# Kernel optimization log

Measured on AMD Instinct MI355X. Metric: run time of the kernel, lower is better.

The kernel has to match this reference:

```python
import jax, jax.numpy as jnp
import numpy as np

NUM_HEADS = 16

def setup_inputs() -> dict:
    key = jax.random.key(0)
    ks = jax.random.split(key, 6)
    S, B, D = 2048, 4, 1280
    return {
        "hidden_states": jax.random.normal(ks[0], (S, B, D), dtype=jnp.float32),
        "rotary_pos_emb": jax.random.normal(ks[1], (S, D // NUM_HEADS // 2), dtype=jnp.float32),
        "in_proj_w": jax.random.normal(ks[2], (3 * D, D), dtype=jnp.float32) * 0.02,
        "in_proj_b": jax.random.normal(ks[3], (3 * D,), dtype=jnp.float32) * 0.02,
        "out_proj_w": jax.random.normal(ks[4], (D, D), dtype=jnp.float32) * 0.02,
        "out_proj_b": jax.random.normal(ks[5], (D,), dtype=jnp.float32) * 0.02,
    }

def _rotate_half(x):
    h = x.shape[-1] // 2
    return jnp.concatenate([-x[..., h:], x[..., :h]], axis=-1)

def _apply_rope(t, cos, sin):
    # t: [B,S,H,Dh]; cos/sin: [1,S,1,Dh]. Compute in fp32 like the original.
    orig = t.dtype
    t32 = t.astype(jnp.float32)
    return (t32 * cos + _rotate_half(t32) * sin).astype(orig)

def reference(hidden_states, rotary_pos_emb, in_proj_w, in_proj_b, out_proj_w, out_proj_b):
    S, B, D = hidden_states.shape
    H = NUM_HEADS
    Dh = D // H

    # Fused QKV projection: [S,B,3D]
    qkv = jnp.einsum('sbd,ed->sbe', hidden_states, in_proj_w) + in_proj_b
    qkv = qkv.reshape(S, B, 3, H, Dh).transpose(2, 1, 0, 3, 4)  # [3,B,S,H,Dh]
    q, k, v = qkv[0], qkv[1], qkv[2]

    # RoPE tables: freqs [S, Dh/2] -> tiled to [1,S,1,Dh] (repeat along last dim)
    cos = jnp.tile(jnp.cos(rotary_pos_emb), (1, 2))[None, :, None, :].astype(jnp.float32)
    sin = jnp.tile(jnp.sin(rotary_pos_emb), (1, 2))[None, :, None, :].astype(jnp.float32)
    q = _apply_rope(q, cos, sin)
    k = _apply_rope(k, cos, sin)

    # [B,H,S,Dh]
    q = q.transpose(0, 2, 1, 3)
    k = k.transpose(0, 2, 1, 3)
    v = v.transpose(0, 2, 1, 3)

    scale = 1.0 / np.sqrt(Dh).astype(np.float32)
    scores = jnp.einsum('bhqd,bhkd->bhqk', q, k) * scale
    attn = jax.nn.softmax(scores, axis=-1)
    out = jnp.einsum('bhqk,bhkd->bhqd', attn, v)  # [B,H,S,Dh]

    out = out.transpose(2, 0, 1, 3).reshape(S, B, D)  # [S,B,D]
    return jnp.einsum('sbd,ed->sbe', out, out_proj_w) + out_proj_b
```

## Files before the change

### kernel.cpp

```cpp
#include <hip/hip_runtime.h>
#include <hip/hip_bf16.h>
#include <math.h>

typedef __bf16 bf16x4 __attribute__((ext_vector_type(4)));
typedef __bf16 bf16x8 __attribute__((ext_vector_type(8)));
typedef float  f32x4  __attribute__((ext_vector_type(4)));

#define S_LEN 2048
#define BATCH 4
#define DMODEL 1280
#define NHEAD 16
#define DHEAD 80
#define KDIM 1280

__device__ __forceinline__ f32x4 mfma_bf16(bf16x8 a, bf16x8 b, f32x4 c) {
  return __builtin_amdgcn_mfma_f32_16x16x32_bf16(a, b, c, 0, 0, 0);
}

__device__ __forceinline__ void gload16(const void* g, void* l) {
  __builtin_amdgcn_global_load_lds(
      (const __attribute__((address_space(1))) unsigned int*)g,
      (__attribute__((address_space(3))) unsigned int*)l, 16, 0, 0);
}

__global__ void cast_f32_to_bf16(const float* __restrict__ in,
                                 __bf16* __restrict__ out, int n4) {
  int i = blockIdx.x * 256 + threadIdx.x;
  if (i >= n4) return;
  float4 v = reinterpret_cast<const float4*>(in)[i];
  bf16x4 o;
  o[0] = (__bf16)v.x; o[1] = (__bf16)v.y; o[2] = (__bf16)v.z; o[3] = (__bf16)v.w;
  reinterpret_cast<bf16x4*>(out)[i] = o;
}

__global__ void build_sincos(const float* __restrict__ rot,
                             float* __restrict__ ctab, float* __restrict__ stab, int n) {
  int i = blockIdx.x * 256 + threadIdx.x;
  if (i >= n) return;
  float v = rot[i];
  ctab[i] = cosf(v);
  stab[i] = sinf(v);
}

__global__ void zero_fill(float* __restrict__ p, int n) {
  int i = blockIdx.x * 256 + threadIdx.x;
  if (i < n) p[i] = 0.0f;
}

__global__ __launch_bounds__(512, 2) void gemm256_qkv(
    const __bf16* __restrict__ A, const __bf16* __restrict__ Bw,
    const float* __restrict__ bias,
    __bf16* __restrict__ qw, __bf16* __restrict__ kw, __bf16* __restrict__ vtw)
{
  __shared__ __align__(1024) char smem[2][65536];
  const int tid = threadIdx.x;
  const int lane = tid & 63;
  const int w = tid >> 6;
  const int lr = lane & 15, lg = lane >> 4;
  const int wr = w >> 2, wc = w & 3;

  const int wg = blockIdx.x;
  const int xcd = wg & 7, idx = wg >> 3;
  const int bx = xcd * 4 + (idx & 3);
  const int by = idx >> 2;
  const int r0 = bx * 256, c0 = by * 256;
  const char* asrc = (const char*)(A + (size_t)r0 * KDIM);
  const char* bsrc = (const char*)(Bw + (size_t)c0 * KDIM);

  f32x4 acc[8][4] = {};

  auto stage = [&](int buf, int kt) {
    const size_t kb = (size_t)kt * 128;
#pragma unroll
    for (int i = 0; i < 8; ++i) {
      const int L = i * 8192 + tid * 16;
      const int r = (L & 32767) >> 7;
      const int coff = (L & 127) ^ ((r & 7) << 4);
      const char* s = (i < 4 ? asrc : bsrc) + (size_t)r * 2560 + kb + coff;
      gload16(s, &smem[buf][L]);
    }
  };

  auto compute = [&](int buf) {
#pragma unroll
    for (int kk = 0; kk < 2; ++kk) {
      bf16x8 af[8], bfr[4];
#pragma unroll
      for (int rt = 0; rt < 8; ++rt) {
        const int row = wr * 128 + rt * 16 + lr;
        af[rt] = *reinterpret_cast<const bf16x8*>(
            &smem[buf][row * 128 + ((kk * 64 + lg * 16) ^ ((row & 7) << 4))]);
      }
#pragma unroll
      for (int ct = 0; ct < 4; ++ct) {
        const int row = wc * 64 + ct * 16 + lr;
        bfr[ct] = *reinterpret_cast<const bf16x8*>(
            &smem[buf][32768 + row * 128 + ((kk * 64 + lg * 16) ^ ((row & 7) << 4))]);
      }
#pragma unroll
      for (int rt = 0; rt < 8; ++rt)
#pragma unroll
        for (int ct = 0; ct < 4; ++ct)
          acc[rt][ct] = mfma_bf16(af[rt], bfr[ct], acc[rt][ct]);
    }
  };

  stage(0, 0);
  asm volatile("s_waitcnt vmcnt(0)" ::: "memory");
  __builtin_amdgcn_s_barrier();
  __builtin_amdgcn_sched_barrier(0);

  for (int t = 0; t < 20; ++t) {
    const int buf = t & 1;
    if (t < 19) stage(buf ^ 1, t + 1);
    compute(buf);
    __builtin_amdgcn_sched_barrier(0);
    asm volatile("s_waitcnt vmcnt(0)" ::: "memory");
    __builtin_amdgcn_sched_barrier(0);
    __builtin_amdgcn_s_barrier();
    __builtin_amdgcn_sched_barrier(0);
  }

  const int which = c0 / DMODEL;
  float biasr[4];
#pragma unroll
  for (int ct = 0; ct < 4; ++ct) biasr[ct] = bias[c0 + wc * 64 + ct * 16 + lr];

#pragma unroll
  for (int ct = 0; ct < 4; ++ct) {
    const int c = c0 + wc * 64 + ct * 16 + lr;
    const int ee = c - which * DMODEL;
    const int h = ee / DHEAD;
    const int dh = ee - h * DHEAD;
#pragma unroll
    for (int rt = 0; rt < 8; ++rt)
#pragma unroll
      for (int j = 0; j < 4; ++j) {
        const int r = r0 + wr * 128 + rt * 16 + lg * 4 + j;
        const int s = r >> 2, b = r & 3;
        const __bf16 bv = (__bf16)(acc[rt][ct][j] + biasr[ct]);
        if (which == 0)
          qw[((size_t)(b * NHEAD + h) * S_LEN + s) * DHEAD + dh] = bv;
        else if (which == 1)
          kw[((size_t)(b * NHEAD + h) * S_LEN + s) * DHEAD + dh] = bv;
        else {
          const int sp = (s & ~31) | ((s & 12) << 1) | ((s & 16) >> 2) | (s & 3);
          vtw[((size_t)(b * NHEAD + h) * DHEAD + dh) * S_LEN + sp] = bv;
        }
      }
  }
}

template <int MODE>
__global__ __launch_bounds__(256) void gemm_bt(
    const __bf16* __restrict__ A, const __bf16* __restrict__ Bw,
    const float* __restrict__ bias, float* __restrict__ outf)
{
  __shared__ __align__(16) char smem[2][2][16384];
  const int tid = threadIdx.x;
  const int lane = tid & 63;
  const int w = tid >> 6;
  const int lr = lane & 15, lg = lane >> 4;
  const int rowblk = (w >> 1) * 64, colblk = (w & 1) * 64;
  const int sxz = (lane & 7) << 4;

  const int wg = blockIdx.x;
  const int xcd = wg & 7, idx = wg >> 3;
  const int bx = xcd * 8 + (idx & 7);
  const int by = idx >> 3;
  const int r0 = bx * 128;
  const int c0 = by * 128;
  const char* asrc = (const char*)(A + (size_t)r0 * KDIM);
  const char* bsrc = (const char*)(Bw + (size_t)c0 * KDIM);

  f32x4 acc[4][4] = {};

  auto stage = [&](int buf, int kt) {
    const size_t kb = (size_t)kt * 128;
#pragma unroll
    for (int i = 0; i < 4; ++i) {
      int L = i * 4096 + tid * 16;
      int r = L >> 7;
      int coff = (L & 127) ^ ((r & 7) << 4);
      gload16(asrc + (size_t)r * 2560 + kb + coff, &smem[buf][0][L]);
      gload16(bsrc + (size_t)r * 2560 + kb + coff, &smem[buf][1][L]);
    }
  };

  auto compute = [&](int buf) {
#pragma unroll
    for (int kk = 0; kk < 2; ++kk) {
      const int cb = (kk * 64 + lg * 16) ^ sxz;
      bf16x8 af[4], bfr[4];
#pragma unroll
      for (int rf = 0; rf < 4; ++rf)
        af[rf] = *reinterpret_cast<const bf16x8*>(&smem[buf][0][(rowblk + rf * 16 + lr) * 128 + cb]);
#pragma unroll
      for (int cf = 0; cf < 4; ++cf)
        bfr[cf] = *reinterpret_cast<const bf16x8*>(&smem[buf][1][(colblk + cf * 16 + lr) * 128 + cb]);
#pragma unroll
      for (int rf = 0; rf < 4; ++rf)
#pragma unroll
        for (int cf = 0; cf < 4; ++cf)
          acc[rf][cf] = mfma_bf16(af[rf], bfr[cf], acc[rf][cf]);
    }
  };

  stage(0, 0);
  asm volatile("s_waitcnt vmcnt(0)" ::: "memory");
  __builtin_amdgcn_s_barrier();
  __builtin_amdgcn_sched_barrier(0);

  for (int t = 0; t < 20; ++t) {
    const int buf = t & 1;
    if (t < 19) {
      stage(buf ^ 1, t + 1);
      asm volatile("s_waitcnt vmcnt(8)" ::: "memory");
    } else {
      asm volatile("s_waitcnt vmcnt(0)" ::: "memory");
    }
    __builtin_amdgcn_sched_barrier(0);
    __builtin_amdgcn_s_barrier();
    __builtin_amdgcn_sched_barrier(0);

    compute(buf);

    __builtin_amdgcn_sched_barrier(0);
    __builtin_amdgcn_s_barrier();
    __builtin_amdgcn_sched_barrier(0);
  }

  float biasr[4];
#pragma unroll
  for (int cf = 0; cf < 4; ++cf) biasr[cf] = bias[c0 + colblk + cf * 16 + lr];

#pragma unroll
  for (int rf = 0; rf < 4; ++rf)
#pragma unroll
    for (int cf = 0; cf < 4; ++cf) {
      const int c = c0 + colblk + cf * 16 + lr;
#pragma unroll
      for (int j = 0; j < 4; ++j) {
        const int r = r0 + rowblk + rf * 16 + lg * 4 + j;
        outf[(size_t)r * DMODEL + c] = acc[rf][cf][j] + biasr[cf];
      }
    }
}

__global__ void rope_kernel(__bf16* __restrict__ qw, __bf16* __restrict__ kw,
                            const float* __restrict__ ctab, const float* __restrict__ stab,
                            float qscale)
{
  int idx = blockIdx.x * 256 + threadIdx.x;
  const int j = idx % 10;
  int rest = idx / 10;
  const int s = rest & (S_LEN - 1);
  rest >>= 11;
  const int bh = rest & 63;
  const int isk = rest >> 6;
  __bf16* base = (isk ? kw : qw) + ((size_t)bh * S_LEN + s) * DHEAD;
  const float4 c4 = *reinterpret_cast<const float4*>(ctab + s * 40 + j * 4);
  const float4 s4 = *reinterpret_cast<const float4*>(stab + s * 40 + j * 4);
  bf16x4 a = *reinterpret_cast<bf16x4*>(base + j * 4);
  bf16x4 b = *reinterpret_cast<bf16x4*>(base + 40 + j * 4);
  const float m = isk ? 1.0f : qscale;
  const float cc[4] = {c4.x, c4.y, c4.z, c4.w};
  const float ss[4] = {s4.x, s4.y, s4.z, s4.w};
#pragma unroll
  for (int t = 0; t < 4; ++t) {
    float fa = (float)a[t], fb = (float)b[t];
    a[t] = (__bf16)((fa * cc[t] - fb * ss[t]) * m);
    b[t] = (__bf16)((fb * cc[t] + fa * ss[t]) * m);
  }
  *reinterpret_cast<bf16x4*>(base + j * 4) = a;
  *reinterpret_cast<bf16x4*>(base + 40 + j * 4) = b;
}

__global__ __launch_bounds__(256, 3) void attn_kernel(
    const __bf16* __restrict__ qw, const __bf16* __restrict__ kw,
    const __bf16* __restrict__ vtw, __bf16* __restrict__ ow,
    const float* __restrict__ zp)
{
  __shared__ __align__(1024) char smem[2][24576];

  const int tid = threadIdx.x;
  const int lane = tid & 63;
  const int w = tid >> 6;
  const int lr = lane & 15, lg = lane >> 4;

  const int wg = blockIdx.x;
  const int local = wg >> 3;
  const int bh = (wg & 7) * 8 + (local >> 4);
  const int qt = local & 15;

  const char* qbase = (const char*)(qw + ((size_t)bh * S_LEN + qt * 128) * DHEAD);
  const char* kbase = (const char*)(kw + (size_t)bh * S_LEN * DHEAD);
  const char* vbase = (const char*)(vtw + (size_t)bh * DHEAD * S_LEN);
  const char* zpb = (const char*)zp;

  bf16x8 z8, one8;
#pragma unroll
  for (int i = 0; i < 8; ++i) { z8[i] = (__bf16)0.0f; one8[i] = (__bf16)1.0f; }

  bf16x8 aq[2][3];
#pragma unroll
  for (int m = 0; m < 2; ++m) {
    const char* rp = qbase + (size_t)(w * 32 + m * 16 + lr) * 160;
    aq[m][0] = *reinterpret_cast<const bf16x8*>(rp + lg * 16);
    aq[m][1] = *reinterpret_cast<const bf16x8*>(rp + 64 + lg * 16);
    aq[m][2] = (lg < 2) ? *reinterpret_cast<const bf16x8*>(rp + 128 + lg * 16) : z8;
  }

  const char* src[6];
  size_t step[6];
#pragma unroll
  for (int i = 0; i < 6; ++i) {
    const int s = w * 6 + i;
    if (s < 12) {
      const int ks = s >> 2, n = s & 3;
      if (ks == 2 && lg >= 2) { src[i] = zpb + lane * 16; step[i] = 0; }
      else { src[i] = kbase + (size_t)(n * 16 + lr) * 160 + ks * 64 + lg * 16; step[i] = 64 * 160; }
    } else {
      const int v = s - 12, mf = v >> 1, ks2 = v & 1;
      if (mf == 5) { src[i] = zpb + lane * 16; step[i] = 0; }
      else { src[i] = vbase + (size_t)(mf * 16 + lr) * 4096 + (size_t)(ks2 * 32 + lg * 8) * 2; step[i] = 128; }
    }
  }

  auto stage = [&](int buf) {
#pragma unroll
    for (int i = 0; i < 6; ++i) {
      gload16(src[i], &smem[buf][(w * 6 + i) * 1024]);
      src[i] += step[i];
    }
  };

  f32x4 accO[5][2] = {};
  f32x4 accD[2] = {};

  stage(0);
  asm volatile("s_waitcnt vmcnt(0)" ::: "memory");
  __builtin_amdgcn_s_barrier();
  __builtin_amdgcn_sched_barrier(0);

  for (int t = 0; t < 32; ++t) {
    const int buf = t & 1;
    if (t < 31) {
      stage(buf ^ 1);
      asm volatile("s_waitcnt vmcnt(6)" ::: "memory");
    } else {
      asm volatile("s_waitcnt vmcnt(0)" ::: "memory");
    }
    __builtin_amdgcn_sched_barrier(0);
    __builtin_amdgcn_s_barrier();
    __builtin_amdgcn_sched_barrier(0);

    const char* Kb = smem[buf];
    const char* Vb = smem[buf] + 12288;

    f32x4 sc[2][4] = {};
#pragma unroll
    for (int n = 0; n < 4; ++n) {
      bf16x8 af0 = *reinterpret_cast<const bf16x8*>(Kb + (0 * 4 + n) * 1024 + lane * 16);
      bf16x8 af1 = *reinterpret_cast<const bf16x8*>(Kb + (1 * 4 + n) * 1024 + lane * 16);
      bf16x8 af2 = *reinterpret_cast<const bf16x8*>(Kb + (2 * 4 + n) * 1024 + lane * 16);
#pragma unroll
      for (int m = 0; m < 2; ++m) {
        sc[m][n] = mfma_bf16(af0, aq[m][0], sc[m][n]);
        sc[m][n] = mfma_bf16(af1, aq[m][1], sc[m][n]);
        sc[m][n] = mfma_bf16(af2, aq[m][2], sc[m][n]);
      }
    }

    bf16x8 bp[2][2];
#pragma unroll
    for (int m = 0; m < 2; ++m)
#pragma unroll
      for (int n = 0; n < 4; ++n) {
#pragma unroll
        for (int j = 0; j < 4; ++j)
          bp[m][n >> 1][(n & 1) * 4 + j] = (__bf16)__builtin_amdgcn_exp2f(sc[m][n][j]);
      }

#pragma unroll
    for (int ks2 = 0; ks2 < 2; ++ks2) {
#pragma unroll
      for (int mf = 0; mf < 5; ++mf) {
        bf16x8 av = *reinterpret_cast<const bf16x8*>(Vb + (mf * 2 + ks2) * 1024 + lane * 16);
        accO[mf][0] = mfma_bf16(av, bp[0][ks2], accO[mf][0]);
        accO[mf][1] = mfma_bf16(av, bp[1][ks2], accO[mf][1]);
      }
      accD[0] = mfma_bf16(one8, bp[0][ks2], accD[0]);
      accD[1] = mfma_bf16(one8, bp[1][ks2], accD[1]);
    }

    __builtin_amdgcn_sched_barrier(0);
    __builtin_amdgcn_s_barrier();
    __builtin_amdgcn_sched_barrier(0);
  }

  __syncthreads();

  float rinv[2];
#pragma unroll
  for (int m = 0; m < 2; ++m) rinv[m] = 1.0f / accD[m][0];

  char* sOut = smem[0];
#pragma unroll
  for (int mf = 0; mf < 5; ++mf)
#pragma unroll
    for (int m = 0; m < 2; ++m) {
      bf16x4 o4;
#pragma unroll
      for (int j = 0; j < 4; ++j) o4[j] = (__bf16)(accO[mf][m][j] * rinv[m]);
      *reinterpret_cast<bf16x4*>(sOut + (size_t)(w * 32 + m * 16 + lr) * 160 + (mf * 16 + lg * 4) * 2) = o4;
    }
  __syncthreads();

  const int b = bh >> 4, h = bh & 15;
#pragma unroll
  for (int i = 0; i < 5; ++i) {
    int c = i * 256 + tid;
    int row = c / 10, slot = c - row * 10;
    int token = (qt * 128 + row) * 4 + b;
    *reinterpret_cast<bf16x8*>((char*)ow + (size_t)token * 2560 + h * 160 + slot * 16) =
        *reinterpret_cast<const bf16x8*>(sOut + row * 160 + slot * 16);
  }
}

extern "C" void kernel_launch(void* const* d_in, const int* in_sizes, int n_in,
                              void* d_out, int out_size, void* d_ws, size_t ws_size,
                              hipStream_t stream)
{
  const float* hidden = (const float*)d_in[0];
  const float* rot    = (const float*)d_in[1];
  const float* w1     = (const float*)d_in[2];
  const float* b1     = (const float*)d_in[3];
  const float* w2     = (const float*)d_in[4];
  const float* b2     = (const float*)d_in[5];
  float* out = (float*)d_out;

  char* ws = (char*)d_ws;
  __bf16* Xbf  = (__bf16*)(ws);
  __bf16* W1bf = (__bf16*)(ws + 20971520);
  __bf16* W2bf = (__bf16*)(ws + 30801920);
  float*  ctab = (float*)(ws + 34078720);
  float*  stab = (float*)(ws + 34406400);
  __bf16* qwp  = (__bf16*)(ws + 34734080);
  __bf16* kwp  = (__bf16*)(ws + 55705600);
  __bf16* vtwp = (__bf16*)(ws + 76677120);
  __bf16* owp  = (__bf16*)(ws + 97648640);
  float*  zp   = (float*)(ws + 118620160);

  cast_f32_to_bf16<<<10240, 256, 0, stream>>>(hidden, Xbf, 2621440);
  cast_f32_to_bf16<<<4800, 256, 0, stream>>>(w1, W1bf, 1228800);
  cast_f32_to_bf16<<<1600, 256, 0, stream>>>(w2, W2bf, 409600);
  build_sincos<<<320, 256, 0, stream>>>(rot, ctab, stab, 81920);
  zero_fill<<<4, 256, 0, stream>>>(zp, 1024);

  gemm256_qkv<<<480, 512, 0, stream>>>(Xbf, W1bf, b1, qwp, kwp, vtwp);

  const float qscale = 1.4426950408889634f / sqrtf(80.0f);
  rope_kernel<<<10240, 256, 0, stream>>>(qwp, kwp, ctab, stab, qscale);

  attn_kernel<<<1024, 256, 0, stream>>>(qwp, kwp, vtwp, owp, zp);

  gemm_bt<1><<<640, 256, 0, stream>>>(owp, W2bf, b2, out);
}
```

Baseline: 276.3 us.

## Interleave QKV GEMM global-to-LDS loads with split MFMA phases

```diff
diff --git a/kernel.cpp b/kernel.cpp
--- a/kernel.cpp
+++ b/kernel.cpp
@@ -69,53 +69,107 @@
 
   f32x4 acc[8][4] = {};
 
-  auto stage = [&](int buf, int kt) {
-    const size_t kb = (size_t)kt * 128;
-#pragma unroll
-    for (int i = 0; i < 8; ++i) {
-      const int L = i * 8192 + tid * 16;
-      const int r = (L & 32767) >> 7;
-      const int coff = (L & 127) ^ ((r & 7) << 4);
-      const char* s = (i < 4 ? asrc : bsrc) + (size_t)r * 2560 + kb + coff;
-      gload16(s, &smem[buf][L]);
-    }
+  const char* gsrc[8];
+  int gdst[8];
+#pragma unroll
+  for (int i = 0; i < 4; ++i) {
+    const int d = 32768 + wc * 8192 + i * 2048 + wr * 1024 + lane * 16;
+    const int r = (d - 32768) >> 7;
+    const int coff = (d & 127) ^ ((r & 7) << 4);
+    gdst[i] = d;
+    gsrc[i] = bsrc + (size_t)r * 2560 + coff;
+  }
+#pragma unroll
+  for (int i = 0; i < 4; ++i) {
+    const int d = wr * 16384 + i * 4096 + wc * 1024 + lane * 16;
+    const int r = d >> 7;
+    const int coff = (d & 127) ^ ((r & 7) << 4);
+    gdst[4 + i] = d;
+    gsrc[4 + i] = asrc + (size_t)r * 2560 + coff;
+  }
+
+  auto issue = [&](int buf, int i) {
+    gload16(gsrc[i], &smem[buf][gdst[i]]);
+    gsrc[i] += 128;
   };
 
-  auto compute = [&](int buf) {
-#pragma unroll
-    for (int kk = 0; kk < 2; ++kk) {
-      bf16x8 af[8], bfr[4];
-#pragma unroll
-      for (int rt = 0; rt < 8; ++rt) {
-        const int row = wr * 128 + rt * 16 + lr;
-        af[rt] = *reinterpret_cast<const bf16x8*>(
-            &smem[buf][row * 128 + ((kk * 64 + lg * 16) ^ ((row & 7) << 4))]);
-      }
-#pragma unroll
-      for (int ct = 0; ct < 4; ++ct) {
-        const int row = wc * 64 + ct * 16 + lr;
-        bfr[ct] = *reinterpret_cast<const bf16x8*>(
-            &smem[buf][32768 + row * 128 + ((kk * 64 + lg * 16) ^ ((row & 7) << 4))]);
-      }
-#pragma unroll
-      for (int rt = 0; rt < 8; ++rt)
-#pragma unroll
-        for (int ct = 0; ct < 4; ++ct)
-          acc[rt][ct] = mfma_bf16(af[rt], bfr[ct], acc[rt][ct]);
+  auto ldA = [&](bf16x8* af, const char* Ab, int rtbase, int kk) {
+#pragma unroll
+    for (int i = 0; i < 4; ++i) {
+      const int row = wr * 128 + (rtbase + i) * 16 + lr;
+      af[i] = *reinterpret_cast<const bf16x8*>(
+          &Ab[row * 128 + ((kk * 64 + lg * 16) ^ ((row & 7) << 4))]);
     }
   };
-
-  stage(0, 0);
+  auto ldB = [&](bf16x8* bfr, const char* Bb, int kk) {
+#pragma unroll
+    for (int ct = 0; ct < 4; ++ct) {
+      const int row = wc * 64 + ct * 16 + lr;
+      bfr[ct] = *reinterpret_cast<const bf16x8*>(
+          &Bb[row * 128 + ((kk * 64 + lg * 16) ^ ((row & 7) << 4))]);
+    }
+  };
+
+#pragma unroll
+  for (int i = 0; i < 8; ++i) issue(0, i);
   asm volatile("s_waitcnt vmcnt(0)" ::: "memory");
   __builtin_amdgcn_s_barrier();
   __builtin_amdgcn_sched_barrier(0);
 
   for (int t = 0; t < 20; ++t) {
-    const int buf = t & 1;
-    if (t < 19) stage(buf ^ 1, t + 1);
-    compute(buf);
-    __builtin_amdgcn_sched_barrier(0);
-    asm volatile("s_waitcnt vmcnt(0)" ::: "memory");
+    const int cbuf = t & 1, nbuf = cbuf ^ 1;
+    const char* Ab = smem[cbuf];
+    const char* Bb = smem[cbuf] + 32768;
+    bf16x8 af[4], bfr[4];
+
+    ldA(af, Ab, 0, 0);
+    ldB(bfr, Bb, 0);
+    issue(nbuf, 0); issue(nbuf, 1);
+    __builtin_amdgcn_s_setprio(1);
+#pragma unroll
+    for (int i = 0; i < 4; ++i)
+#pragma unroll
+      for (int ct = 0; ct < 4; ++ct)
+        acc[i][ct] = mfma_bf16(af[i], bfr[ct], acc[i][ct]);
+    __builtin_amdgcn_s_setprio(0);
+    __builtin_amdgcn_sched_barrier(0);
+    asm volatile("s_waitcnt vmcnt(2)" ::: "memory");
+    __builtin_amdgcn_sched_barrier(0);
+    __builtin_amdgcn_s_barrier();
+    __builtin_amdgcn_sched_barrier(0);
+
+    ldA(af, Ab, 4, 0);
+    issue(nbuf, 2); issue(nbuf, 3);
+    __builtin_amdgcn_s_setprio(1);
+#pragma unroll
+    for (int i = 0; i < 4; ++i)
+#pragma unroll
+      for (int ct = 0; ct < 4; ++ct)
+        acc[4 + i][ct] = mfma_bf16(af[i], bfr[ct], acc[4 + i][ct]);
+    __builtin_amdgcn_s_setprio(0);
+
+    ldA(af, Ab, 0, 1);
+    ldB(bfr, Bb, 1);
+    issue(nbuf, 4); issue(nbuf, 5);
+    __builtin_amdgcn_s_setprio(1);
+#pragma unroll
+    for (int i = 0; i < 4; ++i)
+#pragma unroll
+      for (int ct = 0; ct < 4; ++ct)
+        acc[i][ct] = mfma_bf16(af[i], bfr[ct], acc[i][ct]);
+    __builtin_amdgcn_s_setprio(0);
+
+    ldA(af, Ab, 4, 1);
+    issue(nbuf, 6); issue(nbuf, 7);
+    __builtin_amdgcn_s_setprio(1);
+#pragma unroll
+    for (int i = 0; i < 4; ++i)
+#pragma unroll
+      for (int ct = 0; ct < 4; ++ct)
+        acc[4 + i][ct] = mfma_bf16(af[i], bfr[ct], acc[4 + i][ct]);
+    __builtin_amdgcn_s_setprio(0);
+    __builtin_amdgcn_sched_barrier(0);
+    asm volatile("s_waitcnt vmcnt(2)" ::: "memory");
     __builtin_amdgcn_sched_barrier(0);
     __builtin_amdgcn_s_barrier();
     __builtin_amdgcn_sched_barrier(0);
```

Measured after the change: 272.0 us. About the same (-1.6%).

## Replace 256x256 double-buffered QKV GEMM with 128x128 single-buffered tiles

Applied to the files above, without the earlier changes.

```diff
diff --git a/kernel.cpp b/kernel.cpp
--- a/kernel.cpp
+++ b/kernel.cpp
@@ -47,98 +47,82 @@
   if (i < n) p[i] = 0.0f;
 }
 
-__global__ __launch_bounds__(512, 2) void gemm256_qkv(
+__global__ __launch_bounds__(256, 4) void gemm_qkv128(
     const __bf16* __restrict__ A, const __bf16* __restrict__ Bw,
     const float* __restrict__ bias,
     __bf16* __restrict__ qw, __bf16* __restrict__ kw, __bf16* __restrict__ vtw)
 {
-  __shared__ __align__(1024) char smem[2][65536];
+  __shared__ __align__(1024) char smem[32768];
   const int tid = threadIdx.x;
   const int lane = tid & 63;
   const int w = tid >> 6;
   const int lr = lane & 15, lg = lane >> 4;
-  const int wr = w >> 2, wc = w & 3;
+  const int wr = w >> 1, wc = w & 1;
 
   const int wg = blockIdx.x;
   const int xcd = wg & 7, idx = wg >> 3;
-  const int bx = xcd * 4 + (idx & 3);
-  const int by = idx >> 2;
-  const int r0 = bx * 256, c0 = by * 256;
+  const int bx = xcd * 8 + (idx & 7);
+  const int by = idx >> 3;
+  const int r0 = bx * 128, c0 = by * 128;
   const char* asrc = (const char*)(A + (size_t)r0 * KDIM);
   const char* bsrc = (const char*)(Bw + (size_t)c0 * KDIM);
 
-  f32x4 acc[8][4] = {};
-
-  auto stage = [&](int buf, int kt) {
-    const size_t kb = (size_t)kt * 128;
+  f32x4 acc[4][4] = {};
+
+  for (int t = 0; t < 20; ++t) {
+    const size_t kb = (size_t)t * 128;
 #pragma unroll
     for (int i = 0; i < 8; ++i) {
-      const int L = i * 8192 + tid * 16;
-      const int r = (L & 32767) >> 7;
+      const int L = i * 4096 + tid * 16;
+      const int r = (L & 16383) >> 7;
       const int coff = (L & 127) ^ ((r & 7) << 4);
-      const char* s = (i < 4 ? asrc : bsrc) + (size_t)r * 2560 + kb + coff;
-      gload16(s, &smem[buf][L]);
-    }
-  };
-
-  auto compute = [&](int buf) {
+      const char* s = (L < 16384 ? asrc : bsrc) + (size_t)r * 2560 + kb + coff;
+      gload16(s, &smem[L]);
+    }
+    __syncthreads();
+
 #pragma unroll
     for (int kk = 0; kk < 2; ++kk) {
-      bf16x8 af[8], bfr[4];
-#pragma unroll
-      for (int rt = 0; rt < 8; ++rt) {
-        const int row = wr * 128 + rt * 16 + lr;
-        af[rt] = *reinterpret_cast<const bf16x8*>(
-            &smem[buf][row * 128 + ((kk * 64 + lg * 16) ^ ((row & 7) << 4))]);
-      }
-#pragma unroll
-      for (int ct = 0; ct < 4; ++ct) {
-        const int row = wc * 64 + ct * 16 + lr;
-        bfr[ct] = *reinterpret_cast<const bf16x8*>(
-            &smem[buf][32768 + row * 128 + ((kk * 64 + lg * 16) ^ ((row & 7) << 4))]);
-      }
-#pragma unroll
-      for (int rt = 0; rt < 8; ++rt)
-#pragma unroll
-        for (int ct = 0; ct < 4; ++ct)
-          acc[rt][ct] = mfma_bf16(af[rt], bfr[ct], acc[rt][ct]);
-    }
-  };
-
-  stage(0, 0);
-  asm volatile("s_waitcnt vmcnt(0)" ::: "memory");
-  __builtin_amdgcn_s_barrier();
-  __builtin_amdgcn_sched_barrier(0);
-
-  for (int t = 0; t < 20; ++t) {
-    const int buf = t & 1;
-    if (t < 19) stage(buf ^ 1, t + 1);
-    compute(buf);
-    __builtin_amdgcn_sched_barrier(0);
-    asm volatile("s_waitcnt vmcnt(0)" ::: "memory");
-    __builtin_amdgcn_sched_barrier(0);
-    __builtin_amdgcn_s_barrier();
-    __builtin_amdgcn_sched_barrier(0);
+      bf16x8 af[4], bfr[4];
+#pragma unroll
+      for (int rf = 0; rf < 4; ++rf) {
+        const int row = wr * 64 + rf * 16 + lr;
+        af[rf] = *reinterpret_cast<const bf16x8*>(
+            &smem[row * 128 + ((kk * 64 + lg * 16) ^ ((row & 7) << 4))]);
+      }
+#pragma unroll
+      for (int cf = 0; cf < 4; ++cf) {
+        const int row = wc * 64 + cf * 16 + lr;
+        bfr[cf] = *reinterpret_cast<const bf16x8*>(
+            &smem[16384 + row * 128 + ((kk * 64 + lg * 16) ^ ((row & 7) << 4))]);
+      }
+#pragma unroll
+      for (int rf = 0; rf < 4; ++rf)
+#pragma unroll
+        for (int cf = 0; cf < 4; ++cf)
+          acc[rf][cf] = mfma_bf16(af[rf], bfr[cf], acc[rf][cf]);
+    }
+    __syncthreads();
   }
 
   const int which = c0 / DMODEL;
   float biasr[4];
 #pragma unroll
-  for (int ct = 0; ct < 4; ++ct) biasr[ct] = bias[c0 + wc * 64 + ct * 16 + lr];
-
-#pragma unroll
-  for (int ct = 0; ct < 4; ++ct) {
-    const int c = c0 + wc * 64 + ct * 16 + lr;
+  for (int cf = 0; cf < 4; ++cf) biasr[cf] = bias[c0 + wc * 64 + cf * 16 + lr];
+
+#pragma unroll
+  for (int cf = 0; cf < 4; ++cf) {
+    const int c = c0 + wc * 64 + cf * 16 + lr;
     const int ee = c - which * DMODEL;
     const int h = ee / DHEAD;
     const int dh = ee - h * DHEAD;
 #pragma unroll
-    for (int rt = 0; rt < 8; ++rt)
+    for (int rf = 0; rf < 4; ++rf)
 #pragma unroll
       for (int j = 0; j < 4; ++j) {
-        const int r = r0 + wr * 128 + rt * 16 + lg * 4 + j;
+        const int r = r0 + wr * 64 + rf * 16 + lg * 4 + j;
         const int s = r >> 2, b = r & 3;
-        const __bf16 bv = (__bf16)(acc[rt][ct][j] + biasr[ct]);
+        const __bf16 bv = (__bf16)(acc[rf][cf][j] + biasr[cf]);
         if (which == 0)
           qw[((size_t)(b * NHEAD + h) * S_LEN + s) * DHEAD + dh] = bv;
         else if (which == 1)
@@ -458,7 +442,7 @@
   build_sincos<<<320, 256, 0, stream>>>(rot, ctab, stab, 81920);
   zero_fill<<<4, 256, 0, stream>>>(zp, 1024);
 
-  gemm256_qkv<<<480, 512, 0, stream>>>(Xbf, W1bf, b1, qwp, kwp, vtwp);
+  gemm_qkv128<<<1920, 256, 0, stream>>>(Xbf, W1bf, b1, qwp, kwp, vtwp);
 
   const float qscale = 1.4426950408889634f / sqrtf(80.0f);
   rope_kernel<<<10240, 256, 0, stream>>>(qwp, kwp, ctab, stab, qscale);
```

Result: no change. 275.0 us (-0.5%).

## Restructure QKV GEMM main loop into phased ping-pong schedule with interleaved loads

Applied to the files above, without the earlier changes.

```diff
diff --git a/kernel.cpp b/kernel.cpp
--- a/kernel.cpp
+++ b/kernel.cpp
@@ -22,6 +22,11 @@
       (const __attribute__((address_space(1))) unsigned int*)g,
       (__attribute__((address_space(3))) unsigned int*)l, 16, 0, 0);
 }
+
+#define SB0 __builtin_amdgcn_sched_barrier(0)
+#define BARRIER __builtin_amdgcn_s_barrier()
+#define LGKM0 do { asm volatile("s_waitcnt lgkmcnt(0)" ::: "memory"); SB0; } while (0)
+#define VM2   do { SB0; asm volatile("s_waitcnt vmcnt(2)" ::: "memory"); SB0; } while (0)
 
 __global__ void cast_f32_to_bf16(const float* __restrict__ in,
                                  __bf16* __restrict__ out, int n4) {
@@ -47,7 +52,7 @@
   if (i < n) p[i] = 0.0f;
 }
 
-__global__ __launch_bounds__(512, 2) void gemm256_qkv(
+__global__ __launch_bounds__(512, 2) void gemm_qkv256(
     const __bf16* __restrict__ A, const __bf16* __restrict__ Bw,
     const float* __restrict__ bias,
     __bf16* __restrict__ qw, __bf16* __restrict__ kw, __bf16* __restrict__ vtw)
@@ -67,58 +72,112 @@
   const char* asrc = (const char*)(A + (size_t)r0 * KDIM);
   const char* bsrc = (const char*)(Bw + (size_t)c0 * KDIM);
 
+  const int lrow8 = lane >> 3;
+  const int lsl = (lane & 7) ^ lrow8;
+  const char* aSrcB = asrc + (size_t)(wr * 128 + wc * 32 + lrow8) * 2560 + lsl * 16;
+  const char* bSrcB = bsrc + (size_t)(wc * 64 + wr * 32 + lrow8) * 2560 + lsl * 16;
+  const int aDstR = wr * 128 + wc * 32;
+  const int bDstR = wc * 64 + wr * 32;
+
+  auto issueA = [&](int buf, int kt, int pair) {
+#pragma unroll
+    for (int q = 0; q < 2; ++q) {
+      const int li = pair * 2 + q;
+      gload16(aSrcB + (size_t)kt * 128 + (size_t)li * 8 * 2560,
+              &smem[buf][(aDstR + li * 8) * 128 + lane * 16]);
+    }
+  };
+  auto issueB = [&](int buf, int kt, int pair) {
+#pragma unroll
+    for (int q = 0; q < 2; ++q) {
+      const int li = pair * 2 + q;
+      gload16(bSrcB + (size_t)kt * 128 + (size_t)li * 8 * 2560,
+              &smem[buf][32768 + (bDstR + li * 8) * 128 + lane * 16]);
+    }
+  };
+
   f32x4 acc[8][4] = {};
-
-  auto stage = [&](int buf, int kt) {
-    const size_t kb = (size_t)kt * 128;
-#pragma unroll
-    for (int i = 0; i < 8; ++i) {
-      const int L = i * 8192 + tid * 16;
-      const int r = (L & 32767) >> 7;
-      const int coff = (L & 127) ^ ((r & 7) << 4);
-      const char* s = (i < 4 ? asrc : bsrc) + (size_t)r * 2560 + kb + coff;
-      gload16(s, &smem[buf][L]);
-    }
-  };
-
-  auto compute = [&](int buf) {
-#pragma unroll
-    for (int kk = 0; kk < 2; ++kk) {
-      bf16x8 af[8], bfr[4];
-#pragma unroll
-      for (int rt = 0; rt < 8; ++rt) {
-        const int row = wr * 128 + rt * 16 + lr;
-        af[rt] = *reinterpret_cast<const bf16x8*>(
-            &smem[buf][row * 128 + ((kk * 64 + lg * 16) ^ ((row & 7) << 4))]);
-      }
-#pragma unroll
-      for (int ct = 0; ct < 4; ++ct) {
-        const int row = wc * 64 + ct * 16 + lr;
-        bfr[ct] = *reinterpret_cast<const bf16x8*>(
-            &smem[buf][32768 + row * 128 + ((kk * 64 + lg * 16) ^ ((row & 7) << 4))]);
-      }
-#pragma unroll
-      for (int rt = 0; rt < 8; ++rt)
-#pragma unroll
-        for (int ct = 0; ct < 4; ++ct)
-          acc[rt][ct] = mfma_bf16(af[rt], bfr[ct], acc[rt][ct]);
-    }
-  };
-
-  stage(0, 0);
+  bf16x8 af[4], bfr[4];
+
+  auto ldsA = [&](const char* Sb, int kk, int rtb) {
+#pragma unroll
+    for (int i = 0; i < 4; ++i) {
+      const int row = wr * 128 + (rtb + i) * 16 + lr;
+      af[i] = *reinterpret_cast<const bf16x8*>(
+          &Sb[row * 128 + ((kk * 64 + lg * 16) ^ ((row & 7) << 4))]);
+    }
+  };
+  auto ldsB = [&](const char* Sb, int kk) {
+#pragma unroll
+    for (int ct = 0; ct < 4; ++ct) {
+      const int row = wc * 64 + ct * 16 + lr;
+      bfr[ct] = *reinterpret_cast<const bf16x8*>(
+          &Sb[32768 + row * 128 + ((kk * 64 + lg * 16) ^ ((row & 7) << 4))]);
+    }
+  };
+  auto mfma16 = [&](int rtb) {
+    __builtin_amdgcn_s_setprio(1);
+#pragma unroll
+    for (int i = 0; i < 4; ++i)
+#pragma unroll
+      for (int ct = 0; ct < 4; ++ct)
+        acc[rtb + i][ct] = mfma_bf16(af[i], bfr[ct], acc[rtb + i][ct]);
+    __builtin_amdgcn_s_setprio(0);
+  };
+
+  issueA(0, 0, 0); issueA(0, 0, 1);
+  issueB(0, 0, 0); issueB(0, 0, 1);
+  issueB(1, 1, 0);
   asm volatile("s_waitcnt vmcnt(0)" ::: "memory");
-  __builtin_amdgcn_s_barrier();
-  __builtin_amdgcn_sched_barrier(0);
-
-  for (int t = 0; t < 20; ++t) {
-    const int buf = t & 1;
-    if (t < 19) stage(buf ^ 1, t + 1);
-    compute(buf);
-    __builtin_amdgcn_sched_barrier(0);
-    asm volatile("s_waitcnt vmcnt(0)" ::: "memory");
-    __builtin_amdgcn_sched_barrier(0);
-    __builtin_amdgcn_s_barrier();
-    __builtin_amdgcn_sched_barrier(0);
+  BARRIER; SB0;
+
+  const char* S0 = smem[0];
+  const char* S1 = smem[1];
+
+  for (int it = 0; it < 10; ++it) {
+    const int ta = 2 * it, tb = 2 * it + 1;
+    ldsA(S0, 0, 0); ldsB(S0, 0);
+    issueB(1, tb, 1);
+    SB0; BARRIER; LGKM0;
+    mfma16(0);
+    SB0; BARRIER; SB0;
+    ldsA(S0, 0, 4);
+    issueA(1, tb, 0);
+    SB0; BARRIER; LGKM0;
+    mfma16(4);
+    SB0; BARRIER; SB0;
+    ldsA(S0, 1, 0); ldsB(S0, 1);
+    issueA(1, tb, 1);
+    SB0; BARRIER; LGKM0;
+    mfma16(0);
+    SB0; BARRIER; SB0;
+    ldsA(S0, 1, 4);
+    issueB(0, ta + 2, 0);
+    VM2;
+    BARRIER; LGKM0;
+    mfma16(4);
+    SB0; BARRIER; SB0;
+    ldsA(S1, 0, 0); ldsB(S1, 0);
+    issueB(0, ta + 2, 1);
+    SB0; BARRIER; LGKM0;
+    mfma16(0);
+    SB0; BARRIER; SB0;
+    ldsA(S1, 0, 4);
+    issueA(0, ta + 2, 0);
+    SB0; BARRIER; LGKM0;
+    mfma16(4);
+    SB0; BARRIER; SB0;
+    ldsA(S1, 1, 0); ldsB(S1, 1);
+    issueA(0, ta + 2, 1);
+    SB0; BARRIER; LGKM0;
+    mfma16(0);
+    SB0; BARRIER; SB0;
+    ldsA(S1, 1, 4);
+    issueB(1, tb + 2, 0);
+    VM2;
+    BARRIER; LGKM0;
+    mfma16(4);
+    SB0; BARRIER; SB0;
   }
 
   const int which = c0 / DMODEL;
@@ -458,7 +517,7 @@
   build_sincos<<<320, 256, 0, stream>>>(rot, ctab, stab, 81920);
   zero_fill<<<4, 256, 0, stream>>>(zp, 1024);
 
-  gemm256_qkv<<<480, 512, 0, stream>>>(Xbf, W1bf, b1, qwp, kwp, vtwp);
+  gemm_qkv256<<<480, 512, 0, stream>>>(Xbf, W1bf, b1, qwp, kwp, vtwp);
 
   const float qscale = 1.4426950408889634f / sqrtf(80.0f);
   rope_kernel<<<10240, 256, 0, stream>>>(qwp, kwp, ctab, stab, qscale);
```

Result: no change. 274.1 us (-0.8%).
